# Kernel tuning notes

Hardware: AMD Instinct MI355X
Metric: run time of the kernel (lower is better)

The kernel has to match this reference:

```python
import jax, jax.numpy as jnp
import numpy as np

N = 10000
E = 320000
D = 64


def setup_inputs() -> dict:
    key = jax.random.key(0)
    k1, k2, k3 = jax.random.split(key, 3)
    z = jax.random.normal(k1, (N, D), dtype=jnp.float32)
    edge_index = jax.random.randint(k2, (2, E), 0, N, dtype=jnp.int64)
    W = jax.random.normal(k3, (D, D), dtype=jnp.float32) * (1.0 / np.sqrt(D))
    b = jnp.zeros((D,), dtype=jnp.float32)
    return {"z": z, "edge_index": edge_index, "W": W, "b": b}


def reference(z, edge_index, W, b):
    n = z.shape[0]
    # GCNConv defaults: add self-loops, symmetric normalization D^-1/2 A D^-1/2
    self_loop = jnp.arange(n, dtype=edge_index.dtype)
    row = jnp.concatenate([edge_index[0], self_loop])  # source nodes
    col = jnp.concatenate([edge_index[1], self_loop])  # destination nodes
    deg = jax.ops.segment_sum(jnp.ones_like(col, dtype=z.dtype), col, num_segments=n)
    dinv = jnp.where(deg > 0, jax.lax.rsqrt(deg), 0.0)
    norm = dinv[row] * dinv[col]                        # [E+N]
    h = z @ W                                           # [N, D] linear transform
    msg = h[row] * norm[:, None]                        # gather + scale
    agg = jax.ops.segment_sum(msg, col, num_segments=n) + b  # scatter-add + bias
    zr = jax.nn.relu(agg)
    return zr @ zr.T                                    # [N, N] reconstructed adjacency
```

## Files before the change

kernel.cpp:

```cpp
#include <hip/hip_runtime.h>
#include <math.h>

#define NN 10000
#define NE 320000
#define DD 64
#define TILE 128
#define NTILE 79
#define NPAD (NTILE * TILE)
#define PADROWS (NPAD - NN)

typedef __bf16 bf16x8 __attribute__((ext_vector_type(8)));
typedef float f32x4 __attribute__((ext_vector_type(4)));

#define OFF_CNT    0
#define OFF_FILL   40064
#define OFF_ROWPTR 80128
#define OFF_SRC    120192
#define OFF_DINV   1400192
#define OFF_H      1440256
#define OFF_ZR1    4000256
#define OFF_ZR2    5294592

__global__ void init_kernel(int* __restrict__ cnt, int* __restrict__ fill,
                            unsigned short* __restrict__ zr1,
                            unsigned short* __restrict__ zr2) {
    int tid = blockIdx.x * 256 + threadIdx.x;
    if (tid < NN) { cnt[tid] = 0; fill[tid] = 0; }
    if (tid < PADROWS * DD) {
        zr1[NN * DD + tid] = 0;
        zr2[NN * DD + tid] = 0;
    }
}

__global__ void count_kernel(const int* __restrict__ ei, int* __restrict__ cnt) {
    int e = blockIdx.x * 256 + threadIdx.x;
    if (e < NE) atomicAdd(&cnt[ei[NE + e]], 1);
}

__global__ void dinv_kernel(const int* __restrict__ cnt, float* __restrict__ dinv) {
    int i = blockIdx.x * 256 + threadIdx.x;
    if (i < NN) dinv[i] = rsqrtf((float)cnt[i] + 1.0f);
}

__global__ __launch_bounds__(256) void scan_kernel(const int* __restrict__ cnt,
                                                   int* __restrict__ rowptr) {
    __shared__ int partial[256];
    const int t = threadIdx.x;
    const int base = t * 40;
    int s = 0;
#pragma unroll 4
    for (int i = 0; i < 40; i++) {
        int idx = base + i;
        if (idx < NN) s += cnt[idx];
    }
    partial[t] = s;
    __syncthreads();
    for (int off = 1; off < 256; off <<= 1) {
        int v = (t >= off) ? partial[t - off] : 0;
        __syncthreads();
        partial[t] += v;
        __syncthreads();
    }
    int run = (t == 0) ? 0 : partial[t - 1];
    for (int i = 0; i < 40; i++) {
        int idx = base + i;
        if (idx < NN) { rowptr[idx] = run; run += cnt[idx]; }
    }
    if (t == 255) rowptr[NN] = partial[255];
}

__global__ void fill_kernel(const int* __restrict__ ei,
                            const int* __restrict__ rowptr,
                            int* __restrict__ fill, int* __restrict__ srcrow) {
    int e = blockIdx.x * 256 + threadIdx.x;
    if (e >= NE) return;
    int c = ei[NE + e];
    int pos = rowptr[c] + atomicAdd(&fill[c], 1);
    srcrow[pos] = ei[e];
}

__global__ __launch_bounds__(256) void h_kernel(const float* __restrict__ z,
                                                const float* __restrict__ W,
                                                float* __restrict__ h) {
    __shared__ float Ws[64 * 64];
    __shared__ float zs[4 * 64];
    const int tid = threadIdx.x;
    const int rbase = blockIdx.x * 4;
#pragma unroll
    for (int i = 0; i < 16; i++) Ws[i * 256 + tid] = W[i * 256 + tid];
    zs[tid] = z[rbase * DD + tid];
    __syncthreads();
    const int r = tid >> 6, d = tid & 63;
    float acc = 0.0f;
#pragma unroll
    for (int k = 0; k < 64; k++) acc = fmaf(zs[r * 64 + k], Ws[k * 64 + d], acc);
    h[(rbase + r) * DD + d] = acc;
}

__global__ __launch_bounds__(256) void agg_kernel(const int* __restrict__ rowptr,
                                                  const int* __restrict__ srcrow,
                                                  const float* __restrict__ dinv,
                                                  const float* __restrict__ h,
                                                  const float* __restrict__ b,
                                                  __bf16* __restrict__ zr1,
                                                  __bf16* __restrict__ zr2) {
    const int lane = threadIdx.x & 63;
    const int n = blockIdx.x * 4 + (threadIdx.x >> 6);
    if (n >= NN) return;
    int s = __builtin_amdgcn_readfirstlane(rowptr[n]);
    int e = __builtin_amdgcn_readfirstlane(rowptr[n + 1]);
    const float dc = dinv[n];
    float acc = 0.0f;
    int i = s;
    for (; i + 1 < e; i += 2) {
        int r0 = __builtin_amdgcn_readfirstlane(srcrow[i]);
        int r1 = __builtin_amdgcn_readfirstlane(srcrow[i + 1]);
        float n0 = dinv[r0] * dc, n1 = dinv[r1] * dc;
        float h0 = h[r0 * DD + lane], h1 = h[r1 * DD + lane];
        acc = fmaf(h0, n0, acc);
        acc = fmaf(h1, n1, acc);
    }
    for (; i < e; i++) {
        int r = __builtin_amdgcn_readfirstlane(srcrow[i]);
        acc = fmaf(h[r * DD + lane], dinv[r] * dc, acc);
    }
    acc = fmaf(h[n * DD + lane], dc * dc, acc) + b[lane];
    acc = acc > 0.0f ? acc : 0.0f;
    __bf16 hi = (__bf16)acc;
    float rem = acc - (float)hi;
    zr1[n * DD + lane] = hi;
    zr2[n * DD + lane] = (__bf16)rem;
}

__global__ __launch_bounds__(256) void gemm_kernel(const __bf16* __restrict__ z1,
                                                   const __bf16* __restrict__ z2,
                                                   float* __restrict__ C) {
    const int tid = threadIdx.x;
    const int lane = tid & 63;
    const int w = tid >> 6;
    const int wr = w >> 1, wc = w & 1;
    const int m16 = lane & 15;
    const int kq = lane >> 4;
    const int rbase = blockIdx.y * TILE + wr * 64;
    const int cbase = blockIdx.x * TILE + wc * 64;

    f32x4 acc[4][4] = {};

    for (int kk = 0; kk < 2; kk++) {
        const int ko = kk * 32 + kq * 8;
        bf16x8 a1[4], a2[4], b1[4], b2[4];
#pragma unroll
        for (int t = 0; t < 4; t++) {
            const int ar = rbase + t * 16 + m16;
            const int br = cbase + t * 16 + m16;
            a1[t] = *(const bf16x8*)&z1[ar * DD + ko];
            a2[t] = *(const bf16x8*)&z2[ar * DD + ko];
            b1[t] = *(const bf16x8*)&z1[br * DD + ko];
            b2[t] = *(const bf16x8*)&z2[br * DD + ko];
        }
#pragma unroll
        for (int mt = 0; mt < 4; mt++)
#pragma unroll
            for (int nt = 0; nt < 4; nt++) {
                acc[mt][nt] = __builtin_amdgcn_mfma_f32_16x16x32_bf16(a2[mt], b1[nt], acc[mt][nt], 0, 0, 0);
                acc[mt][nt] = __builtin_amdgcn_mfma_f32_16x16x32_bf16(a1[mt], b2[nt], acc[mt][nt], 0, 0, 0);
                acc[mt][nt] = __builtin_amdgcn_mfma_f32_16x16x32_bf16(a1[mt], b1[nt], acc[mt][nt], 0, 0, 0);
            }
    }

#pragma unroll
    for (int mt = 0; mt < 4; mt++) {
        const int row0 = rbase + mt * 16 + kq * 4;
#pragma unroll
        for (int nt = 0; nt < 4; nt++) {
            const int col = cbase + nt * 16 + m16;
            if (col < NN) {
#pragma unroll
                for (int r = 0; r < 4; r++) {
                    const int row = row0 + r;
                    if (row < NN) C[(size_t)row * NN + col] = acc[mt][nt][r];
                }
            }
        }
    }
}

extern "C" void kernel_launch(void* const* d_in, const int* in_sizes, int n_in,
                              void* d_out, int out_size, void* d_ws, size_t ws_size,
                              hipStream_t stream) {
    const float* z = (const float*)d_in[0];
    const int* ei = (const int*)d_in[1];
    const float* W = (const float*)d_in[2];
    const float* b = (const float*)d_in[3];
    float* C = (float*)d_out;

    char* ws = (char*)d_ws;
    int* cnt = (int*)(ws + OFF_CNT);
    int* fill = (int*)(ws + OFF_FILL);
    int* rowptr = (int*)(ws + OFF_ROWPTR);
    int* srcrow = (int*)(ws + OFF_SRC);
    float* dinv = (float*)(ws + OFF_DINV);
    float* h = (float*)(ws + OFF_H);
    __bf16* zr1 = (__bf16*)(ws + OFF_ZR1);
    __bf16* zr2 = (__bf16*)(ws + OFF_ZR2);

    init_kernel<<<(NN + 255) / 256, 256, 0, stream>>>(cnt, fill,
                                                      (unsigned short*)zr1,
                                                      (unsigned short*)zr2);
    count_kernel<<<(NE + 255) / 256, 256, 0, stream>>>(ei, cnt);
    dinv_kernel<<<(NN + 255) / 256, 256, 0, stream>>>(cnt, dinv);
    scan_kernel<<<1, 256, 0, stream>>>(cnt, rowptr);
    fill_kernel<<<(NE + 255) / 256, 256, 0, stream>>>(ei, rowptr, fill, srcrow);
    h_kernel<<<NN / 4, 256, 0, stream>>>(z, W, h);
    agg_kernel<<<(NN + 3) / 4, 256, 0, stream>>>(rowptr, srcrow, dinv, h, b, zr1, zr2);

    dim3 grid(NTILE, NTILE);
    gemm_kernel<<<grid, 256, 0, stream>>>(zr1, zr2, C);
}
```

Measured before the change: 548.4 us.

## Exploit symmetry of zr·zrᵀ by computing only upper-triangular tiles

The output is symmetric, so the GEMM grid now covers only upper-triangular tile pairs, mapped from a linear block index via a sqrt-based triangular decode. Off-diagonal blocks write their tile and also its transpose using vectorized float4 stores. This roughly halves the MFMA work and operand loads, but the kernel is dominated by writing the 400MB output, so store traffic is unchanged and the transposed stores have a different access pattern.

New measurement: 544.6 us. Within noise of the previous version (-0.7%).

```diff
diff --git a/kernel.cpp b/kernel.cpp
--- a/kernel.cpp
+++ b/kernel.cpp
@@ -8,6 +8,7 @@
 #define NTILE 79
 #define NPAD (NTILE * TILE)
 #define PADROWS (NPAD - NN)
+#define NPAIRS (NTILE * (NTILE + 1) / 2)
 
 typedef __bf16 bf16x8 __attribute__((ext_vector_type(8)));
 typedef float f32x4 __attribute__((ext_vector_type(4)));
@@ -135,14 +136,21 @@
 __global__ __launch_bounds__(256) void gemm_kernel(const __bf16* __restrict__ z1,
                                                    const __bf16* __restrict__ z2,
                                                    float* __restrict__ C) {
+    const int t = blockIdx.x;
+    const float ff = (float)(2 * NTILE + 1);
+    int bi = (int)((ff - sqrtf(ff * ff - 8.0f * (float)t)) * 0.5f);
+    while ((bi + 1) * NTILE - ((bi + 1) * bi) / 2 <= t) bi++;
+    while (bi * NTILE - (bi * (bi - 1)) / 2 > t) bi--;
+    const int bj = bi + (t - (bi * NTILE - (bi * (bi - 1)) / 2));
+
     const int tid = threadIdx.x;
     const int lane = tid & 63;
     const int w = tid >> 6;
     const int wr = w >> 1, wc = w & 1;
     const int m16 = lane & 15;
     const int kq = lane >> 4;
-    const int rbase = blockIdx.y * TILE + wr * 64;
-    const int cbase = blockIdx.x * TILE + wc * 64;
+    const int rbase = bi * TILE + wr * 64;
+    const int cbase = bj * TILE + wc * 64;
 
     f32x4 acc[4][4] = {};
 
@@ -150,13 +158,13 @@
         const int ko = kk * 32 + kq * 8;
         bf16x8 a1[4], a2[4], b1[4], b2[4];
 #pragma unroll
-        for (int t = 0; t < 4; t++) {
-            const int ar = rbase + t * 16 + m16;
-            const int br = cbase + t * 16 + m16;
-            a1[t] = *(const bf16x8*)&z1[ar * DD + ko];
-            a2[t] = *(const bf16x8*)&z2[ar * DD + ko];
-            b1[t] = *(const bf16x8*)&z1[br * DD + ko];
-            b2[t] = *(const bf16x8*)&z2[br * DD + ko];
+        for (int tt = 0; tt < 4; tt++) {
+            const int ar = rbase + tt * 16 + m16;
+            const int br = cbase + tt * 16 + m16;
+            a1[tt] = *(const bf16x8*)&z1[ar * DD + ko];
+            a2[tt] = *(const bf16x8*)&z2[ar * DD + ko];
+            b1[tt] = *(const bf16x8*)&z1[br * DD + ko];
+            b2[tt] = *(const bf16x8*)&z2[br * DD + ko];
         }
 #pragma unroll
         for (int mt = 0; mt < 4; mt++)
@@ -179,6 +187,21 @@
                 for (int r = 0; r < 4; r++) {
                     const int row = row0 + r;
                     if (row < NN) C[(size_t)row * NN + col] = acc[mt][nt][r];
+                }
+            }
+        }
+    }
+
+    if (bi != bj) {
+#pragma unroll
+        for (int mt = 0; mt < 4; mt++) {
+            const int tcol0 = rbase + mt * 16 + kq * 4;
+            if (tcol0 < NN) {
+#pragma unroll
+                for (int nt = 0; nt < 4; nt++) {
+                    const int trow = cbase + nt * 16 + m16;
+                    if (trow < NN)
+                        *(f32x4*)&C[(size_t)trow * NN + tcol0] = acc[mt][nt];
                 }
             }
         }
@@ -214,6 +237,5 @@
     h_kernel<<<NN / 4, 256, 0, stream>>>(z, W, h);
     agg_kernel<<<(NN + 3) / 4, 256, 0, stream>>>(rowptr, srcrow, dinv, h, b, zr1, zr2);
 
-    dim3 grid(NTILE, NTILE);
-    gemm_kernel<<<grid, 256, 0, stream>>>(zr1, zr2, C);
-}
+    gemm_kernel<<<NPAIRS, 256, 0, stream>>>(zr1, zr2, C);
+}
```
